# Kernel tuning notes

Measured on AMD Instinct MI355X. Metric: run time of the kernel, lower is better.

The kernel has to match this reference:

```python
import jax, jax.numpy as jnp
import numpy as np

N_NODES = 50000
N_EDGES = 800000
IN_CH = 128
HID = 64
OUT_CH = 2
NEG_SLOPE = 0.2


def gcn_conv(x, src, dst, deg_isqrt, W, b):
    # PyG GCNConv: x @ W, symmetric normalization with self-loops, scatter-add, + bias
    h = x @ W  # [N, HID]
    norm = deg_isqrt[src] * deg_isqrt[dst]  # [E+N]
    msg = h[src] * norm[:, None]  # gather + scale
    out = jax.ops.segment_sum(msg, dst, num_segments=x.shape[0])
    return out + b


def setup_inputs() -> dict:
    key = jax.random.key(0)
    ks = jax.random.split(key, 16)
    glorot = lambda k, i, o: jax.random.normal(k, (i, o), jnp.float32) * jnp.sqrt(2.0 / (i + o))
    inp = {
        "node_features": jax.random.normal(ks[0], (N_NODES, IN_CH), jnp.float32),
        "edge_index": jax.random.randint(ks[1], (2, N_EDGES), 0, N_NODES, jnp.int64 if jax.config.jax_enable_x64 else jnp.int32),
        "fc1_W": glorot(ks[2], IN_CH, 32), "fc1_b": jnp.zeros((32,), jnp.float32),
        "fc2_W": glorot(ks[3], 32, HID), "fc2_b": jnp.zeros((HID,), jnp.float32),
        "conv1_W": glorot(ks[4], HID, HID), "conv1_b": jnp.zeros((HID,), jnp.float32),
        "conv2_W": glorot(ks[5], HID, HID), "conv2_b": jnp.zeros((HID,), jnp.float32),
        "conv3_W": glorot(ks[6], HID, HID), "conv3_b": jnp.zeros((HID,), jnp.float32),
        "conv4_W": glorot(ks[7], HID, HID), "conv4_b": jnp.zeros((HID,), jnp.float32),
        "final_W": glorot(ks[8], HID, OUT_CH), "final_b": jnp.zeros((OUT_CH,), jnp.float32),
    }
    return inp


def reference(node_features, edge_index, fc1_W, fc1_b, fc2_W, fc2_b,
              conv1_W, conv1_b, conv2_W, conv2_b, conv3_W, conv3_b,
              conv4_W, conv4_b, final_W, final_b):
    N = node_features.shape[0]
    # add self-loops once (shared by all conv layers)
    loops = jnp.arange(N, dtype=edge_index.dtype)
    src = jnp.concatenate([edge_index[0], loops])
    dst = jnp.concatenate([edge_index[1], loops])
    deg = jax.ops.segment_sum(jnp.ones_like(dst, jnp.float32), dst, num_segments=N)
    deg_isqrt = jnp.where(deg > 0, jax.lax.rsqrt(jnp.maximum(deg, 1.0)), 0.0)

    lrelu = lambda x: jnp.where(x >= 0, x, NEG_SLOPE * x)

    x = jax.nn.relu(node_features @ fc1_W + fc1_b) @ fc2_W + fc2_b  # fc stack
    out1 = lrelu(gcn_conv(x, src, dst, deg_isqrt, conv1_W, conv1_b))
    out2 = lrelu(gcn_conv(out1, src, dst, deg_isqrt, conv2_W, conv2_b)) + out1
    out3 = lrelu(gcn_conv(out2, src, dst, deg_isqrt, conv3_W, conv3_b))
    out4 = gcn_conv(out3, src, dst, deg_isqrt, conv4_W, conv4_b) + out2
    return out4 @ final_W + final_b
```

## Files before the change

kernel.cpp:

```cpp
#include <hip/hip_runtime.h>

#define NN 50000
#define NHALF 25000
#define NE 800000
#define HIST_BLOCKS ((NE + 255) / 256)
#define FILL_BLOCKS HIST_BLOCKS
#define FC_BLOCKS 1024

typedef unsigned short u16;
typedef unsigned int u32;

__device__ inline float rlf(float v, int l) {
    return __int_as_float(__builtin_amdgcn_readlane(__float_as_int(v), l));
}
__device__ inline u16 f2bf(float f) {
    u32 u = __float_as_uint(f);
    u32 r = (u + 0x7FFFu + ((u >> 16) & 1u)) >> 16;
    return (u16)r;
}
__device__ inline float lo16(u32 q) { return __uint_as_float(q << 16); }
__device__ inline float hi16(u32 q) { return __uint_as_float(q & 0xffff0000u); }

__global__ __launch_bounds__(256) void k_hist_foldw(
    const int* __restrict__ dst, int* __restrict__ cnt, u16* __restrict__ rank,
    const float* __restrict__ fc2W, const float* __restrict__ b2,
    const float* __restrict__ c1W, float* __restrict__ W2c,
    float* __restrict__ b2c) {
    if (blockIdx.x < HIST_BLOCKS) {
        int e = blockIdx.x * 256 + threadIdx.x;
        if (e < NE) rank[e] = (u16)atomicAdd(&cnt[dst[e]], 1);
    } else {
        int j = (blockIdx.x - HIST_BLOCKS) * 4 + (threadIdx.x >> 6);
        int c = threadIdx.x & 63;
        if (j < 32) {
            float s = 0.f;
            for (int k = 0; k < 64; ++k) s = fmaf(fc2W[j * 64 + k], c1W[k * 64 + c], s);
            W2c[j * 64 + c] = s;
        } else if (j == 32) {
            float s = 0.f;
            for (int k = 0; k < 64; ++k) s = fmaf(b2[k], c1W[k * 64 + c], s);
            b2c[c] = s;
        }
    }
}

__global__ __launch_bounds__(1024) void k_scan(const int* __restrict__ cnt,
                                               int* __restrict__ rowptr,
                                               float* __restrict__ disq,
                                               u16* __restrict__ Hb) {
    __shared__ int wsum[16];
    __shared__ int carry;
    int t = threadIdx.x, wave = t >> 6, lane = t & 63;
    if (t == 0) { carry = 0; rowptr[0] = 0; }
    if (t < 64) Hb[(size_t)NN * 64 + t] = 0;
    __syncthreads();
    for (int base = 0; base < NN; base += 1024) {
        int i = base + t;
        int x = (i < NN) ? cnt[i] : 0;
        if (i < NN) disq[i] = rsqrtf((float)x + 1.0f);
        for (int off = 1; off < 64; off <<= 1) {
            int y = __shfl_up(x, off, 64);
            if (lane >= off) x += y;
        }
        if (lane == 63) wsum[wave] = x;
        __syncthreads();
        if (wave == 0 && lane < 16) {
            int w = wsum[lane];
            for (int off = 1; off < 16; off <<= 1) {
                int y = __shfl_up(w, off, 16);
                if (lane >= off) w += y;
            }
            wsum[lane] = w;
        }
        __syncthreads();
        int incl = carry + ((wave > 0) ? wsum[wave - 1] : 0) + x;
        if (i < NN) rowptr[i + 1] = incl;
        __syncthreads();
        if (t == 1023) carry = incl;
        __syncthreads();
    }
}

__global__ __launch_bounds__(256) void k_fill_fc(
    const int* __restrict__ src, const int* __restrict__ dst,
    const int* __restrict__ rowptr, const u16* __restrict__ rank,
    u16* __restrict__ esrc,
    const float* __restrict__ nf,
    const float* __restrict__ W1, const float* __restrict__ b1,
    const float* __restrict__ W2c, const float* __restrict__ b2c,
    const float* __restrict__ disq, u16* __restrict__ Hb) {
    if (blockIdx.x >= FC_BLOCKS) {
        int e = (blockIdx.x - FC_BLOCKS) * 256 + threadIdx.x;
        if (e < NE) {
            int d = dst[e];
            int pos = rowptr[d] + (int)rank[e];
            __builtin_nontemporal_store((u16)src[e], &esrc[pos]);
        }
        return;
    }
    int lane = threadIdx.x & 63;
    int c = lane & 31, h = lane >> 5;
    int wid = (blockIdx.x * 256 + threadIdx.x) >> 6;
    int nwaves = (FC_BLOCKS * 256) >> 6;
    float w1[64], w2[32];
    #pragma unroll
    for (int j = 0; j < 64; ++j) w1[j] = W1[(h * 64 + j) * 32 + c];
    #pragma unroll
    for (int j = 0; j < 32; ++j) w2[j] = W2c[j * 64 + lane];
    float b1c = b1[c], b2l = b2c[lane];
    for (int n = wid; n < NN; n += nwaves) {
        float x0 = nf[(size_t)n * 128 + lane];
        float x1 = nf[(size_t)n * 128 + 64 + lane];
        float s0 = 0.f, s1 = 0.f;
        #pragma unroll
        for (int j = 0; j < 32; ++j) {
            float xa = rlf(x0, j), xb = rlf(x1, j);
            float xc = rlf(x0, j + 32), xd = rlf(x1, j + 32);
            s0 = fmaf(h ? xb : xa, w1[j], s0);
            s1 = fmaf(h ? xd : xc, w1[j + 32], s1);
        }
        float s = s0 + s1;
        s += __shfl_xor(s, 32, 64);
        float hv = fmaxf(s + b1c, 0.f);
        float o0 = b2l, o1 = 0.f;
        #pragma unroll
        for (int j = 0; j < 16; ++j) {
            o0 = fmaf(rlf(hv, j), w2[j], o0);
            o1 = fmaf(rlf(hv, j + 16), w2[j + 16], o1);
        }
        Hb[(size_t)n * 64 + lane] = f2bf(disq[n] * (o0 + o1));
    }
}

__global__ __launch_bounds__(256) void k_gemm64(
    const float* __restrict__ X, const float* __restrict__ W,
    const float* __restrict__ disq, u16* __restrict__ Hb) {
    int lane = threadIdx.x & 63;
    int wid = (blockIdx.x * 256 + threadIdx.x) >> 6;
    int nwaves = (gridDim.x * 256) >> 6;
    float wcol[64];
    #pragma unroll
    for (int k = 0; k < 64; ++k) wcol[k] = W[k * 64 + lane];
    for (int n = wid; n < NN; n += nwaves) {
        float xv = X[(size_t)n * 64 + lane];
        float acc = 0.f;
        #pragma unroll
        for (int k = 0; k < 64; ++k) acc = fmaf(rlf(xv, k), wcol[k], acc);
        Hb[(size_t)n * 64 + lane] = f2bf(disq[n] * acc);
    }
}

#define GRPA(J)                                                             \
    {                                                                       \
        int p0 = __builtin_amdgcn_readlane(idx1, (J) + 0);                  \
        int p1 = __builtin_amdgcn_readlane(idx1, (J) + 1);                  \
        int p2 = __builtin_amdgcn_readlane(idx1, (J) + 2);                  \
        int p3 = __builtin_amdgcn_readlane(idx1, (J) + 3);                  \
        int s = (q == 0) ? p0 : ((q == 1) ? p1 : ((q == 2) ? p2 : p3));     \
        uint2 v = *(const uint2*)(Hb + (((size_t)s) << 6) + c4);            \
        a0 += lo16(v.x); a1 += hi16(v.x); a2 += lo16(v.y); a3 += hi16(v.y); \
    }
#define GRPB(J)                                                             \
    {                                                                       \
        int p0 = __builtin_amdgcn_readlane(idx2, (J) + 0);                  \
        int p1 = __builtin_amdgcn_readlane(idx2, (J) + 1);                  \
        int p2 = __builtin_amdgcn_readlane(idx2, (J) + 2);                  \
        int p3 = __builtin_amdgcn_readlane(idx2, (J) + 3);                  \
        int s = (q == 0) ? p0 : ((q == 1) ? p1 : ((q == 2) ? p2 : p3));     \
        uint2 v = *(const uint2*)(Hb + (((size_t)s) << 6) + c4);            \
        g0 += lo16(v.x); g1 += hi16(v.x); g2 += lo16(v.y); g3 += hi16(v.y); \
    }

__global__ __launch_bounds__(256) void k_csr_conv(
    const u16* __restrict__ Hb, const int* __restrict__ rowptr,
    const u16* __restrict__ esrc, const float* __restrict__ disq,
    const float* __restrict__ b, const float* __restrict__ res,
    float* __restrict__ out, int do_lrelu) {
    int lane = threadIdx.x & 63;
    int q = lane >> 4;
    int c4 = (lane & 15) * 4;
    int w = (blockIdx.x * 256 + threadIdx.x) >> 6;
    if (w >= NHALF) return;
    int n1 = w, n2 = w + NHALF;
    int base1 = rowptr[n1], end1 = rowptr[n1 + 1];
    int base2 = rowptr[n2], end2 = rowptr[n2 + 1];
    float a0 = 0.f, a1 = 0.f, a2 = 0.f, a3 = 0.f;
    float g0 = 0.f, g1 = 0.f, g2 = 0.f, g3 = 0.f;
    while (base1 < end1 || base2 < end2) {
        int m1 = min(max(end1 - base1, 0), 64);
        int m2 = min(max(end2 - base2, 0), 64);
        int idx1 = (lane < m1) ? (int)esrc[base1 + lane] : NN;
        int idx2 = (lane < m2) ? (int)esrc[base2 + lane] : NN;
        int m = max(m1, m2);
        int j = 0;
        for (; j + 16 <= m; j += 16) {
            GRPA(j) GRPB(j) GRPA(j + 4) GRPB(j + 4)
            GRPA(j + 8) GRPB(j + 8) GRPA(j + 12) GRPB(j + 12)
        }
        for (; j < m; j += 4) { GRPA(j) GRPB(j) }
        base1 += 64;
        base2 += 64;
    }
    a0 += __shfl_xor(a0, 16, 64); a0 += __shfl_xor(a0, 32, 64);
    a1 += __shfl_xor(a1, 16, 64); a1 += __shfl_xor(a1, 32, 64);
    a2 += __shfl_xor(a2, 16, 64); a2 += __shfl_xor(a2, 32, 64);
    a3 += __shfl_xor(a3, 16, 64); a3 += __shfl_xor(a3, 32, 64);
    g0 += __shfl_xor(g0, 16, 64); g0 += __shfl_xor(g0, 32, 64);
    g1 += __shfl_xor(g1, 16, 64); g1 += __shfl_xor(g1, 32, 64);
    g2 += __shfl_xor(g2, 16, 64); g2 += __shfl_xor(g2, 32, 64);
    g3 += __shfl_xor(g3, 16, 64); g3 += __shfl_xor(g3, 32, 64);
    if (q < 2) {
        int n = (q == 0) ? n1 : n2;
        float e0 = (q == 0) ? a0 : g0;
        float e1 = (q == 0) ? a1 : g1;
        float e2 = (q == 0) ? a2 : g2;
        float e3 = (q == 0) ? a3 : g3;
        uint2 sv = *(const uint2*)(Hb + (((size_t)n) << 6) + c4);
        e0 += lo16(sv.x); e1 += hi16(sv.x); e2 += lo16(sv.y); e3 += hi16(sv.y);
        float dn = disq[n];
        float4 bv = *(const float4*)(b + c4);
        float v0 = dn * e0 + bv.x;
        float v1 = dn * e1 + bv.y;
        float v2 = dn * e2 + bv.z;
        float v3 = dn * e3 + bv.w;
        if (do_lrelu) {
            v0 = (v0 >= 0.f) ? v0 : 0.2f * v0;
            v1 = (v1 >= 0.f) ? v1 : 0.2f * v1;
            v2 = (v2 >= 0.f) ? v2 : 0.2f * v2;
            v3 = (v3 >= 0.f) ? v3 : 0.2f * v3;
        }
        if (res) {
            float4 r = *(const float4*)(res + (((size_t)n) << 6) + c4);
            v0 += r.x; v1 += r.y; v2 += r.z; v3 += r.w;
        }
        float4 o;
        o.x = v0; o.y = v1; o.z = v2; o.w = v3;
        *(float4*)(out + (((size_t)n) << 6) + c4) = o;
    }
}

__global__ __launch_bounds__(256) void k_csr_conv_final(
    const u16* __restrict__ Hb, const int* __restrict__ rowptr,
    const u16* __restrict__ esrc, const float* __restrict__ disq,
    const float* __restrict__ b, const float* __restrict__ res,
    const float* __restrict__ FW, const float* __restrict__ fb,
    float* __restrict__ out) {
    int lane = threadIdx.x & 63;
    int q = lane >> 4;
    int c4 = (lane & 15) * 4;
    int w = (blockIdx.x * 256 + threadIdx.x) >> 6;
    if (w >= NHALF) return;
    int n1 = w, n2 = w + NHALF;
    int base1 = rowptr[n1], end1 = rowptr[n1 + 1];
    int base2 = rowptr[n2], end2 = rowptr[n2 + 1];
    float a0 = 0.f, a1 = 0.f, a2 = 0.f, a3 = 0.f;
    float g0 = 0.f, g1 = 0.f, g2 = 0.f, g3 = 0.f;
    while (base1 < end1 || base2 < end2) {
        int m1 = min(max(end1 - base1, 0), 64);
        int m2 = min(max(end2 - base2, 0), 64);
        int idx1 = (lane < m1) ? (int)esrc[base1 + lane] : NN;
        int idx2 = (lane < m2) ? (int)esrc[base2 + lane] : NN;
        int m = max(m1, m2);
        int j = 0;
        for (; j + 16 <= m; j += 16) {
            GRPA(j) GRPB(j) GRPA(j + 4) GRPB(j + 4)
            GRPA(j + 8) GRPB(j + 8) GRPA(j + 12) GRPB(j + 12)
        }
        for (; j < m; j += 4) { GRPA(j) GRPB(j) }
        base1 += 64;
        base2 += 64;
    }
    a0 += __shfl_xor(a0, 16, 64); a0 += __shfl_xor(a0, 32, 64);
    a1 += __shfl_xor(a1, 16, 64); a1 += __shfl_xor(a1, 32, 64);
    a2 += __shfl_xor(a2, 16, 64); a2 += __shfl_xor(a2, 32, 64);
    a3 += __shfl_xor(a3, 16, 64); a3 += __shfl_xor(a3, 32, 64);
    g0 += __shfl_xor(g0, 16, 64); g0 += __shfl_xor(g0, 32, 64);
    g1 += __shfl_xor(g1, 16, 64); g1 += __shfl_xor(g1, 32, 64);
    g2 += __shfl_xor(g2, 16, 64); g2 += __shfl_xor(g2, 32, 64);
    g3 += __shfl_xor(g3, 16, 64); g3 += __shfl_xor(g3, 32, 64);
    float p0 = 0.f, p1 = 0.f;
    int n = (q == 0) ? n1 : n2;
    if (q < 2) {
        float e0 = (q == 0) ? a0 : g0;
        float e1 = (q == 0) ? a1 : g1;
        float e2 = (q == 0) ? a2 : g2;
        float e3 = (q == 0) ? a3 : g3;
        uint2 sv = *(const uint2*)(Hb + (((size_t)n) << 6) + c4);
        e0 += lo16(sv.x); e1 += hi16(sv.x); e2 += lo16(sv.y); e3 += hi16(sv.y);
        float dn = disq[n];
        float4 bv = *(const float4*)(b + c4);
        float4 r = *(const float4*)(res + (((size_t)n) << 6) + c4);
        float v0 = dn * e0 + bv.x + r.x;
        float v1 = dn * e1 + bv.y + r.y;
        float v2 = dn * e2 + bv.z + r.z;
        float v3 = dn * e3 + bv.w + r.w;
        float4 f01 = *(const float4*)(FW + c4 * 2);
        float4 f23 = *(const float4*)(FW + c4 * 2 + 4);
        p0 = v0 * f01.x + v1 * f01.z + v2 * f23.x + v3 * f23.z;
        p1 = v0 * f01.y + v1 * f01.w + v2 * f23.y + v3 * f23.w;
    }
    for (int off = 1; off < 16; off <<= 1) {
        p0 += __shfl_xor(p0, off, 64);
        p1 += __shfl_xor(p1, off, 64);
    }
    if (lane == 0 || lane == 16) {
        out[n * 2 + 0] = p0 + fb[0];
        out[n * 2 + 1] = p1 + fb[1];
    }
}

extern "C" void kernel_launch(void* const* d_in, const int* in_sizes, int n_in,
                              void* d_out, int out_size, void* d_ws, size_t ws_size,
                              hipStream_t stream) {
    const float* nf   = (const float*)d_in[0];
    const int*   ei   = (const int*)d_in[1];
    const float* fc1W = (const float*)d_in[2];
    const float* fc1b = (const float*)d_in[3];
    const float* fc2W = (const float*)d_in[4];
    const float* fc2b = (const float*)d_in[5];
    const float* cW[4] = {(const float*)d_in[6], (const float*)d_in[8],
                          (const float*)d_in[10], (const float*)d_in[12]};
    const float* cb[4] = {(const float*)d_in[7], (const float*)d_in[9],
                          (const float*)d_in[11], (const float*)d_in[13]};
    const float* fW = (const float*)d_in[14];
    const float* fb = (const float*)d_in[15];
    const int* src = ei;
    const int* dst = ei + NE;

    float* ws     = (float*)d_ws;
    float* disq   = ws;
    int*   cnt    = (int*)(ws + 50048);
    int*   rowptr = cnt + 50048;
    u16*   esrc   = (u16*)(rowptr + 50056);
    u16*   rank   = esrc + 800000;
    float* W2c    = (float*)(rank + 800000);
    float* b2c    = W2c + 2048;
    float* B0     = b2c + 64;
    float* B1     = B0 + (size_t)NN * 64;
    u16*   Hb     = (u16*)(B1 + (size_t)NN * 64);

    hipMemsetAsync(cnt, 0, 50048 * sizeof(int), stream);
    k_hist_foldw<<<HIST_BLOCKS + 9, 256, 0, stream>>>(dst, cnt, rank, fc2W, fc2b,
                                                      cW[0], W2c, b2c);
    k_scan<<<1, 1024, 0, stream>>>(cnt, rowptr, disq, Hb);
    k_fill_fc<<<FC_BLOCKS + FILL_BLOCKS, 256, 0, stream>>>(
        src, dst, rowptr, rank, esrc, nf, fc1W, fc1b, W2c, b2c, disq, Hb);

    const int cgrid = (NHALF * 64 + 255) / 256;

    k_csr_conv<<<cgrid, 256, 0, stream>>>(Hb, rowptr, esrc, disq, cb[0], nullptr, B1, 1);
    k_gemm64<<<1024, 256, 0, stream>>>(B1, cW[1], disq, Hb);
    k_csr_conv<<<cgrid, 256, 0, stream>>>(Hb, rowptr, esrc, disq, cb[1], B1, B0, 1);
    k_gemm64<<<1024, 256, 0, stream>>>(B0, cW[2], disq, Hb);
    k_csr_conv<<<cgrid, 256, 0, stream>>>(Hb, rowptr, esrc, disq, cb[2], nullptr, B1, 1);
    k_gemm64<<<1024, 256, 0, stream>>>(B1, cW[3], disq, Hb);
    k_csr_conv_final<<<cgrid, 256, 0, stream>>>(Hb, rowptr, esrc, disq, cb[3], B0,
                                                fW, fb, (float*)d_out);
}
```

Measured before the change: 303.5 us.

## Fuse next-layer 64x64 GEMM into CSR aggregation epilogue with ping-pong buffers

Removes the separate k_gemm64 launches. Each CSR conv kernel now stages the next layer's weight in shared memory and, after aggregating a node pair, computes the next layer's transformed, normalized bf16 features directly. Because other waves still read the current buffer during the gather, two feature buffers are alternated. This saves three kernel launches and the float round trip through global memory, but adds 16KB of LDS per block and a per-block weight load, which may lower occupancy of the gather kernel.

```diff
diff --git a/kernel.cpp b/kernel.cpp
--- a/kernel.cpp
+++ b/kernel.cpp
@@ -6,6 +6,7 @@
 #define HIST_BLOCKS ((NE + 255) / 256)
 #define FILL_BLOCKS HIST_BLOCKS
 #define FC_BLOCKS 1024
+#define HBSZ ((size_t)(NN + 1) * 64)
 
 typedef unsigned short u16;
 typedef unsigned int u32;
@@ -47,12 +48,14 @@
 __global__ __launch_bounds__(1024) void k_scan(const int* __restrict__ cnt,
                                                int* __restrict__ rowptr,
                                                float* __restrict__ disq,
-                                               u16* __restrict__ Hb) {
+                                               u16* __restrict__ HbA,
+                                               u16* __restrict__ HbB) {
     __shared__ int wsum[16];
     __shared__ int carry;
     int t = threadIdx.x, wave = t >> 6, lane = t & 63;
     if (t == 0) { carry = 0; rowptr[0] = 0; }
-    if (t < 64) Hb[(size_t)NN * 64 + t] = 0;
+    if (t < 64) HbA[(size_t)NN * 64 + t] = 0;
+    else if (t < 128) HbB[(size_t)NN * 64 + (t - 64)] = 0;
     __syncthreads();
     for (int base = 0; base < NN; base += 1024) {
         int i = base + t;
@@ -132,24 +135,6 @@
     }
 }
 
-__global__ __launch_bounds__(256) void k_gemm64(
-    const float* __restrict__ X, const float* __restrict__ W,
-    const float* __restrict__ disq, u16* __restrict__ Hb) {
-    int lane = threadIdx.x & 63;
-    int wid = (blockIdx.x * 256 + threadIdx.x) >> 6;
-    int nwaves = (gridDim.x * 256) >> 6;
-    float wcol[64];
-    #pragma unroll
-    for (int k = 0; k < 64; ++k) wcol[k] = W[k * 64 + lane];
-    for (int n = wid; n < NN; n += nwaves) {
-        float xv = X[(size_t)n * 64 + lane];
-        float acc = 0.f;
-        #pragma unroll
-        for (int k = 0; k < 64; ++k) acc = fmaf(rlf(xv, k), wcol[k], acc);
-        Hb[(size_t)n * 64 + lane] = f2bf(disq[n] * acc);
-    }
-}
-
 #define GRPA(J)                                                             \
     {                                                                       \
         int p0 = __builtin_amdgcn_readlane(idx1, (J) + 0);                  \
@@ -171,11 +156,15 @@
         g0 += lo16(v.x); g1 += hi16(v.x); g2 += lo16(v.y); g3 += hi16(v.y); \
     }
 
-__global__ __launch_bounds__(256) void k_csr_conv(
+__global__ __launch_bounds__(256) void k_csr_fused(
     const u16* __restrict__ Hb, const int* __restrict__ rowptr,
     const u16* __restrict__ esrc, const float* __restrict__ disq,
     const float* __restrict__ b, const float* __restrict__ res,
-    float* __restrict__ out, int do_lrelu) {
+    float* __restrict__ out, const float* __restrict__ Wn,
+    u16* __restrict__ HbN) {
+    __shared__ float sW[64 * 64];
+    for (int i = threadIdx.x; i < 4096; i += 256) sW[i] = Wn[i];
+    __syncthreads();
     int lane = threadIdx.x & 63;
     int q = lane >> 4;
     int c4 = (lane & 15) * 4;
@@ -209,6 +198,7 @@
     g1 += __shfl_xor(g1, 16, 64); g1 += __shfl_xor(g1, 32, 64);
     g2 += __shfl_xor(g2, 16, 64); g2 += __shfl_xor(g2, 32, 64);
     g3 += __shfl_xor(g3, 16, 64); g3 += __shfl_xor(g3, 32, 64);
+    float vv[4] = {0.f, 0.f, 0.f, 0.f};
     if (q < 2) {
         int n = (q == 0) ? n1 : n2;
         float e0 = (q == 0) ? a0 : g0;
@@ -223,20 +213,42 @@
         float v1 = dn * e1 + bv.y;
         float v2 = dn * e2 + bv.z;
         float v3 = dn * e3 + bv.w;
-        if (do_lrelu) {
-            v0 = (v0 >= 0.f) ? v0 : 0.2f * v0;
-            v1 = (v1 >= 0.f) ? v1 : 0.2f * v1;
-            v2 = (v2 >= 0.f) ? v2 : 0.2f * v2;
-            v3 = (v3 >= 0.f) ? v3 : 0.2f * v3;
-        }
+        v0 = (v0 >= 0.f) ? v0 : 0.2f * v0;
+        v1 = (v1 >= 0.f) ? v1 : 0.2f * v1;
+        v2 = (v2 >= 0.f) ? v2 : 0.2f * v2;
+        v3 = (v3 >= 0.f) ? v3 : 0.2f * v3;
         if (res) {
             float4 r = *(const float4*)(res + (((size_t)n) << 6) + c4);
             v0 += r.x; v1 += r.y; v2 += r.z; v3 += r.w;
         }
-        float4 o;
-        o.x = v0; o.y = v1; o.z = v2; o.w = v3;
-        *(float4*)(out + (((size_t)n) << 6) + c4) = o;
-    }
+        vv[0] = v0; vv[1] = v1; vv[2] = v2; vv[3] = v3;
+        if (out) {
+            float4 o;
+            o.x = v0; o.y = v1; o.z = v2; o.w = v3;
+            *(float4*)(out + (((size_t)n) << 6) + c4) = o;
+        }
+    }
+    int cp = (lane & 31) * 2;
+    float o0 = 0.f, o1 = 0.f, o2 = 0.f, o3 = 0.f;
+    #pragma unroll
+    for (int k = 0; k < 32; ++k) {
+        float vA0 = rlf(vv[k & 3], k >> 2);
+        float vB0 = rlf(vv[k & 3], 16 + (k >> 2));
+        float vA1 = rlf(vv[k & 3], (k + 32) >> 2);
+        float vB1 = rlf(vv[k & 3], 16 + ((k + 32) >> 2));
+        float vk0 = (lane < 32) ? vA0 : vB0;
+        float vk1 = (lane < 32) ? vA1 : vB1;
+        float2 w0 = *(const float2*)(sW + k * 64 + cp);
+        float2 w1 = *(const float2*)(sW + (k + 32) * 64 + cp);
+        o0 = fmaf(vk0, w0.x, o0);
+        o1 = fmaf(vk0, w0.y, o1);
+        o2 = fmaf(vk1, w1.x, o2);
+        o3 = fmaf(vk1, w1.y, o3);
+    }
+    int nn = (lane < 32) ? n1 : n2;
+    float dnn = disq[nn];
+    u32 packed = (u32)f2bf(dnn * (o0 + o2)) | ((u32)f2bf(dnn * (o1 + o3)) << 16);
+    *(u32*)(HbN + (((size_t)nn) << 6) + cp) = packed;
 }
 
 __global__ __launch_bounds__(256) void k_csr_conv_final(
@@ -337,23 +349,24 @@
     float* b2c    = W2c + 2048;
     float* B0     = b2c + 64;
     float* B1     = B0 + (size_t)NN * 64;
-    u16*   Hb     = (u16*)(B1 + (size_t)NN * 64);
+    u16*   HbA    = (u16*)(B1 + (size_t)NN * 64);
+    u16*   HbB    = HbA + HBSZ;
 
     hipMemsetAsync(cnt, 0, 50048 * sizeof(int), stream);
     k_hist_foldw<<<HIST_BLOCKS + 9, 256, 0, stream>>>(dst, cnt, rank, fc2W, fc2b,
                                                       cW[0], W2c, b2c);
-    k_scan<<<1, 1024, 0, stream>>>(cnt, rowptr, disq, Hb);
+    k_scan<<<1, 1024, 0, stream>>>(cnt, rowptr, disq, HbA, HbB);
     k_fill_fc<<<FC_BLOCKS + FILL_BLOCKS, 256, 0, stream>>>(
-        src, dst, rowptr, rank, esrc, nf, fc1W, fc1b, W2c, b2c, disq, Hb);
+        src, dst, rowptr, rank, esrc, nf, fc1W, fc1b, W2c, b2c, disq, HbA);
 
     const int cgrid = (NHALF * 64 + 255) / 256;
 
-    k_csr_conv<<<cgrid, 256, 0, stream>>>(Hb, rowptr, esrc, disq, cb[0], nullptr, B1, 1);
-    k_gemm64<<<1024, 256, 0, stream>>>(B1, cW[1], disq, Hb);
-    k_csr_conv<<<cgrid, 256, 0, stream>>>(Hb, rowptr, esrc, disq, cb[1], B1, B0, 1);
-    k_gemm64<<<1024, 256, 0, stream>>>(B0, cW[2], disq, Hb);
-    k_csr_conv<<<cgrid, 256, 0, stream>>>(Hb, rowptr, esrc, disq, cb[2], nullptr, B1, 1);
-    k_gemm64<<<1024, 256, 0, stream>>>(B1, cW[3], disq, Hb);
-    k_csr_conv_final<<<cgrid, 256, 0, stream>>>(Hb, rowptr, esrc, disq, cb[3], B0,
-                                                fW, fb, (float*)d_out);
-}
+    k_csr_fused<<<cgrid, 256, 0, stream>>>(HbA, rowptr, esrc, disq, cb[0],
+                                           nullptr, B1, cW[1], HbB);
+    k_csr_fused<<<cgrid, 256, 0, stream>>>(HbB, rowptr, esrc, disq, cb[1],
+                                           B1, B0, cW[2], HbA);
+    k_csr_fused<<<cgrid, 256, 0, stream>>>(HbA, rowptr, esrc, disq, cb[2],
+                                           nullptr, nullptr, cW[3], HbB);
+    k_csr_conv_final<<<cgrid, 256, 0, stream>>>(HbB, rowptr, esrc, disq, cb[3],
+                                                B0, fW, fb, (float*)d_out);
+}
```

Result: no change. 299.3 us (-1.4%).
